# Optimization experiments

Measured on AMD Instinct MI355X. Metric: run time of the kernel, lower is better.

The kernel has to match this reference:

```python
import jax, jax.numpy as jnp
import numpy as np
from jax import lax

B, N, C, CN, M, H, W = 2, 8192, 64, 64, 16, 180, 240
LN_EPS = 1e-5  # torch nn.LayerNorm([C]) default eps


def setup_inputs():
    key = jax.random.key(0)
    ks = jax.random.split(key, 20)
    x = jax.random.uniform(ks[0], (B, N)) * (W - 1)
    y = jax.random.uniform(ks[1], (B, N)) * (H - 1)
    t = jax.random.uniform(ks[2], (B, N))
    p = jnp.where(jax.random.uniform(ks[3], (B, N)) < 0.5, -1.0, 1.0)
    events = jnp.stack([x, y, t, p], axis=-1)  # [B,N,4]
    s = 0.05
    w = lambda k, shape: jax.random.normal(k, shape) * s
    return {
        "events": events,
        "W_mlp1": w(ks[4], (4, C)),
        "W_pe": w(ks[5], (4, CN)),
        "ln_w": jnp.ones((C,)),
        "ln_b": jnp.zeros((C,)),
        "lx_Wq": w(ks[6], (C, CN)), "lx_Wk": w(ks[7], (C, CN)),
        "lx_Wv": w(ks[8], (C, CN)), "lx_Wsa1": w(ks[9], (CN, 1)),
        "lx_Wsa2": w(ks[10], (CN, C)),
        "gx_Wq": w(ks[11], (C, CN)), "gx_Wk": w(ks[12], (C, CN)),
        "gx_Wv": w(ks[13], (C, CN)), "gx_Wpe": w(ks[14], (C, CN)),
        "gx_Wsa1": w(ks[15], (CN, 1)), "gx_Wsa2": w(ks[16], (CN, C)),
    }


def select_nearest(vect, m):
    # torch: F.pad(left=m//2, right=m//2-1) then unfold(dim=1, size=m, step=1)
    b, n, c = vect.shape
    pad = m // 2
    vp = jnp.pad(vect, ((0, 0), (pad, pad - 1), (0, 0)))
    idx = jnp.arange(n)[:, None] + jnp.arange(m)[None, :]  # [N,M]
    return vp[:, idx, :]  # [B,N,M,C]


def fps(event, npoint):
    # faithful farthest_point_sample_batch; masked_select returns the sampled
    # points in ORIGINAL index order, hence the sort of selected indices.
    b, n, c = event.shape
    bary = jnp.mean(event, axis=1, keepdims=True)
    farthest0 = jnp.argmax(jnp.sum((event - bary) ** 2, -1), axis=1)  # [B]
    dist0 = jnp.full((b, n), 1e10, event.dtype)

    def step(carry, _):
        distance, farthest = carry
        centroid = jnp.take_along_axis(event, farthest[:, None, None], axis=1)
        d = jnp.sum((event - centroid) ** 2, -1)
        distance = jnp.minimum(distance, d)  # distance[dist<distance]=dist
        return (distance, jnp.argmax(distance, axis=1)), farthest

    _, sel = lax.scan(step, (dist0, farthest0), None, length=npoint)
    sel = jnp.sort(sel.T, axis=1)  # [B,npoint], sorted index order
    return jnp.take_along_axis(event, sel[:, :, None], axis=1)  # [B,npoint,C]


def sub_attention(q, k_multi, v_multi, pe, Wsa1, Wsa2):
    # sa = q - k + pe -> Linear(Cn,1) -> softmax over M.
    # The original then computes matmul(scores[B,1,N,M], (v+pe)^T[B,Cn,M,N])
    # and sums over the last axis, which is exactly
    #   scores @ (sum_n (v_multi + pe))  -- computed here without the
    # [B,Cn,N,N] intermediate.
    sa = q[:, :, None, :] - k_multi + pe          # [B,N,M,Cn]
    logits = jnp.squeeze(sa @ Wsa1, -1)           # [B,N,M]
    scores = jax.nn.softmax(logits, axis=-1)
    S = jnp.sum(v_multi + pe, axis=1)             # [B,M,Cn]
    p_attn = jnp.einsum("bnm,bmc->bnc", scores, S)
    return p_attn @ Wsa2                          # [B,N,C]


def layer_norm(x, w, b):
    mu = jnp.mean(x, axis=-1, keepdims=True)
    var = jnp.var(x, axis=-1, keepdims=True)
    return (x - mu) / jnp.sqrt(var + LN_EPS) * w + b


def normalize_nonzero(space):
    # mean/std over nonzero entries (std unbiased, ddof=1 as torch.std)
    mask = space != 0
    cnt = jnp.sum(mask)
    mean = jnp.sum(jnp.where(mask, space, 0.0)) / jnp.maximum(cnt, 1)
    var = jnp.sum(jnp.where(mask, (space - mean) ** 2, 0.0)) / jnp.maximum(cnt - 1, 1)
    std = jnp.sqrt(var)
    centered = jnp.where(mask, space - mean, space)
    safe_std = jnp.where(std > 0, std, 1.0)
    normed = jnp.where(std > 0, centered / safe_std, centered)
    return jnp.where(cnt > 0, normed, space)


def events_to_image(feat, ev, ln_w, ln_b):
    # feat [N,C], ev [N,4]
    h = jax.nn.gelu(layer_norm(feat, ln_w, ln_b), approximate=False)
    xi = jnp.floor(ev[:, 0]).astype(jnp.int32)
    yi = jnp.floor(ev[:, 1]).astype(jnp.int32)
    p = ev[:, 3]
    flat = yi * W + xi
    space = jnp.zeros((H * W, h.shape[1]), h.dtype).at[flat].add(p[:, None] * h)
    return normalize_nonzero(space.reshape(H, W, -1))


def reference(events, W_mlp1, W_pe, ln_w, ln_b,
              lx_Wq, lx_Wk, lx_Wv, lx_Wsa1, lx_Wsa2,
              gx_Wq, gx_Wk, gx_Wv, gx_Wpe, gx_Wsa1, gx_Wsa2):
    b, n, _ = events.shape
    lx_in = events @ W_mlp1                                    # [B,N,C]
    # EventTransformer position encoding: unfold-neighbor differences in raw
    # 4-d event space, then Linear(4,Cn)
    pe = (events[:, :, None, :] - select_nearest(events, M)) @ W_pe  # [B,N,M,Cn]
    # LXformer
    q = lx_in @ lx_Wq
    k = lx_in @ lx_Wk
    v = lx_in @ lx_Wv
    lx_sa = sub_attention(q, select_nearest(k, M), select_nearest(v, M),
                          pe, lx_Wsa1, lx_Wsa2)
    lx_out = lx_in + lx_sa
    # GXformer: FPS-sampled global keys/values, FPS-based position encoding
    pe_g = (lx_out[:, :, None, :] - fps(lx_out, M)[:, None, :, :]) @ gx_Wpe
    qg = lx_out @ gx_Wq
    kg = lx_out @ gx_Wk
    vg = lx_out @ gx_Wv
    k_m = jnp.broadcast_to(fps(kg, M)[:, None], (b, n, M, CN))
    v_m = jnp.broadcast_to(fps(vg, M)[:, None], (b, n, M, CN))
    gx_sa = sub_attention(qg, k_m, v_m, pe_g, gx_Wsa1, gx_Wsa2)
    gx_out = lx_out + gx_sa
    # scatter events to image per batch element
    imgs = jax.vmap(lambda f, e: events_to_image(f, e, ln_w, ln_b))(gx_out, events)
    return jnp.transpose(imgs, (0, 3, 1, 2))  # [B,C,H,W]
```

## Files before the change

kernel.cpp:

```cpp
#include <hip/hip_runtime.h>


typedef unsigned short u16;
typedef unsigned long long ull;

#define NB 8192
#define IMG_H 180
#define IMG_W 240
#define HWPIX (IMG_H*IMG_W)
#define SPB (HWPIX*64)
#define NC (NB*64)

#define TT_AC    0
#define TT_T     16384
#define TT_W1    32768
#define TT_EDGEV 32960
#define TT_EDGEF 35008
#define TT_S     37056
#define TT_SEL   39104
#define TT_CG    45248
#define TT_ESUM  45376
#define TT_STATS 45408
#define TT_SYNC  45440
#define TT_GCNT  45632
#define TT_LXS   45664
#define TT_ZOFF  45376
#define TT_ZCNT  416
#define TT_TOT   45792

__device__ __forceinline__ float bf2f(u16 u){
  union { unsigned int i; float f; } w; w.i = ((unsigned int)u) << 16; return w.f;
}
__device__ __forceinline__ u16 f2bf(float f){
  union { unsigned int i; float f; } w; w.f = f;
  unsigned int x = w.i;
  x += 0x7fffu + ((x >> 16) & 1u);
  return (u16)(x >> 16);
}
__device__ __forceinline__ bool isbf(const void* ev){
  unsigned w3 = ((const unsigned*)ev)[3];
  return !(w3 == 0x3F800000u || w3 == 0xBF800000u);
}
__device__ __forceinline__ float ld(const void* p, int i, bool bf){
  return bf ? bf2f(((const u16*)p)[i]) : ((const float*)p)[i];
}
__device__ __forceinline__ void stout(void* o, long i, float v, bool bf){
  if (bf) ((u16*)o)[i] = f2bf(v); else ((float*)o)[i] = v;
}
__device__ __forceinline__ float waveSum(float v){
#pragma unroll
  for (int m = 1; m < 64; m <<= 1) v += __shfl_xor(v, m, 64);
  return v;
}
__device__ __forceinline__ ull waveMaxU64(ull v){
#pragma unroll
  for (int m = 1; m < 64; m <<= 1){
    ull o = (ull)__shfl_xor((long long)v, m, 64);
    if (o > v) v = o;
  }
  return v;
}
__device__ __forceinline__ ull packPDI(int phase, float d, int n){
  return ((ull)phase << 45) | ((ull)__float_as_uint(d) << 13) | (ull)(8191 - n);
}
__device__ __forceinline__ int unpackI(ull p){ return 8191 - (int)(p & 0x1FFFull); }

__global__ void kW(const void* __restrict__ ev, const void* __restrict__ Wq,
                   const void* __restrict__ Wk, const void* __restrict__ Wpe,
                   const void* __restrict__ w1, float* __restrict__ ws, int tail){
  const bool bf = isbf(ev);
  const int tid = threadIdx.x;
  for (int i = tid; i < TT_ZCNT; i += 256) ws[tail + TT_ZOFF + i] = 0.f;
  if (tid < 64){
    float s1 = 0.f, s2 = 0.f;
    for (int c = 0; c < 64; c++){
      float wc = ld(w1, c, bf);
      s1 += ld(Wq, tid*64 + c, bf) * wc;
      s2 += ld(Wk, tid*64 + c, bf) * wc;
    }
    ws[tail + TT_W1 + tid] = s1;
    ws[tail + TT_W1 + 64 + tid] = s2;
    if (tid < 4){
      float s3 = 0.f;
      for (int c = 0; c < 64; c++) s3 += ld(Wpe, tid*64 + c, bf) * ld(w1, c, bf);
      ws[tail + TT_W1 + 128 + tid] = s3;
    }
  }
}

__global__ void __launch_bounds__(256, 4) kA(const void* __restrict__ ev,
    const void* __restrict__ Wm, const void* __restrict__ Wpe,
    const void* __restrict__ Wv, float* __restrict__ ws,
    int offA, int strA, int tail, int bb0){
  const bool bf = isbf(ev);
  const int bb = bb0 + blockIdx.z;
  const int lane = threadIdx.x & 63, w = threadIdx.x >> 6;
  float* A = ws + offA + (size_t)bb*strA;
  const float wq1 = ws[tail + TT_W1 + lane];
  const float wk1 = ws[tail + TT_W1 + 64 + lane];
  const float wp10 = ws[tail+TT_W1+128], wp11 = ws[tail+TT_W1+129],
              wp12 = ws[tail+TT_W1+130], wp13 = ws[tail+TT_W1+131];
  const float wm0 = ld(Wm, 0*64+lane, bf), wm1 = ld(Wm, 1*64+lane, bf),
              wm2 = ld(Wm, 2*64+lane, bf), wm3 = ld(Wm, 3*64+lane, bf);
  const bool edgeBlk = (blockIdx.x == 0 || blockIdx.x == 1023);
  float se0 = 0.f, se1 = 0.f, se2 = 0.f, se3 = 0.f;
#pragma unroll
  for (int i = 0; i < 2; i++){
    const int n = blockIdx.x*8 + w + 4*i;
    const int e4 = (bb*NB + n)*4;
    float e0 = ld(ev, e4+0, bf), e1 = ld(ev, e4+1, bf),
          e2 = ld(ev, e4+2, bf), e3 = ld(ev, e4+3, bf);
    se0 += e0; se1 += e1; se2 += e2; se3 += e3;
    float lx = e0*wm0 + e1*wm1 + e2*wm2 + e3*wm3;
    float epe = e0*wp10 + e1*wp11 + e2*wp12 + e3*wp13;
    float acv = waveSum(lx * wq1) + epe;
    float tv  = waveSum(lx * wk1) + epe;
    A[n*64 + lane] = lx;
    if (lane == 0){
      ws[tail + TT_AC + bb*8192 + n] = acv;
      ws[tail + TT_T  + bb*8192 + n] = tv;
    }
    if (edgeBlk && (n < 8 || n >= NB-8)){
      int e = (n < 8) ? n : (n - (NB-16));
      float v = 0.f;
      for (int cn = 0; cn < 64; cn++)
        v += __shfl(lx, cn, 64) * ld(Wv, cn*64 + lane, bf);
      float f = e0*ld(Wpe, lane, bf) + e1*ld(Wpe, 64+lane, bf)
              + e2*ld(Wpe, 128+lane, bf) + e3*ld(Wpe, 192+lane, bf);
      ws[tail + TT_EDGEV + bb*1024 + e*64 + lane] = v;
      ws[tail + TT_EDGEF + bb*1024 + e*64 + lane] = f;
    }
  }
  __shared__ float esum[4][4];
  if (lane == 0){ esum[w][0]=se0; esum[w][1]=se1; esum[w][2]=se2; esum[w][3]=se3; }
  __syncthreads();
  if (threadIdx.x < 4)
    atomicAdd(&ws[tail + TT_ESUM + bb*16 + threadIdx.x],
              esum[0][threadIdx.x]+esum[1][threadIdx.x]+esum[2][threadIdx.x]+esum[3][threadIdx.x]);
}

__global__ void __launch_bounds__(64) kB(const void* __restrict__ ev,
    const void* __restrict__ Wm, const void* __restrict__ Wv,
    const void* __restrict__ Wsa2, float* __restrict__ ws, int tail, int bb0){
  const bool bf = isbf(ev);
  const int bb = bb0 + blockIdx.z;
  const int m = blockIdx.x, lane = threadIdx.x;
  float tm = 0.f;
#pragma unroll
  for (int i = 0; i < 4; i++) tm += ws[tail + TT_ESUM + bb*16 + i] * ld(Wm, i*64 + lane, bf);
  float vs0 = 0.f, vs1 = 0.f;
#pragma unroll
  for (int j = 0; j < 64; j += 2){
    vs0 += __shfl(tm, j, 64)   * ld(Wv, j*64 + lane, bf);
    vs1 += __shfl(tm, j+1, 64) * ld(Wv, (j+1)*64 + lane, bf);
  }
  float vsum = vs0 + vs1;
  const int d = m - 8;
  float sv = 0.f, sf = 0.f;
  const float* EV = ws + tail + TT_EDGEV + bb*1024;
  const float* EF = ws + tail + TT_EDGEF + bb*1024;
  if (d < 0){
    for (int e = 16 + d; e < 16; e++){ sv += EV[e*64+lane]; sf += EF[e*64+lane]; }
  } else {
    for (int e = 0; e < d; e++){ sv += EV[e*64+lane]; sf += EF[e*64+lane]; }
  }
  float S = vsum - sv + sf;
  float sw0 = 0.f, sw1 = 0.f;
#pragma unroll
  for (int c = 0; c < 64; c += 2){
    sw0 += __shfl(S, c, 64)   * ld(Wsa2, c*64 + lane, bf);
    sw1 += __shfl(S, c+1, 64) * ld(Wsa2, (c+1)*64 + lane, bf);
  }
  ws[tail + TT_S + bb*1024 + m*64 + lane] = sw0 + sw1;
}

__global__ void __launch_bounds__(256) kC(const void* __restrict__ ev,
    const void* __restrict__ gWk, const void* __restrict__ gWv,
    float* __restrict__ ws,
    int offA, int strA, int offB, int strB, int offC, int strC,
    int tail, int bb0){
  const bool bf = isbf(ev);
  const int bb = bb0 + blockIdx.z;
  float* A = ws + offA + (size_t)bb*strA;
  float* Bp = ws + offB + (size_t)bb*strB;
  float* Cp = ws + offC + (size_t)bb*strC;
  __shared__ float SW_lds[1024];
  __shared__ float WK[4096];
  __shared__ float WV[4096];
  __shared__ float lred[4][64];
  const int tid = threadIdx.x, lane = tid & 63, w = tid >> 6;
  for (int i = tid; i < 1024; i += 256) SW_lds[i] = ws[tail + TT_S + bb*1024 + i];
  for (int i = tid; i < 4096; i += 256){
    WK[i] = ld(gWk, i, bf);
    WV[i] = ld(gWv, i, bf);
  }
  __syncthreads();
  float lxoR[2];
  float lxsum = 0.f;
#pragma unroll
  for (int i = 0; i < 2; i++){
    const int n = blockIdx.x*8 + w + 4*i;
    float lx  = A[n*64 + lane];
    float acn = ws[tail + TT_AC + bb*8192 + n];
    const int m = lane & 15;
    const int j = n + m - 8;
    float tv = (j >= 0 && j < NB) ? ws[tail + TT_T + bb*8192 + j] : 0.f;
    float logit = acn - tv;
    float mx = logit;
#pragma unroll
    for (int k = 1; k < 16; k <<= 1) mx = fmaxf(mx, __shfl_xor(mx, k, 64));
    float ex = expf(logit - mx);
    float sm = ex;
#pragma unroll
    for (int k = 1; k < 16; k <<= 1) sm += __shfl_xor(sm, k, 64);
    float sig = ex / sm;
    float sa = 0.f;
#pragma unroll
    for (int mm = 0; mm < 16; mm++) sa += __shfl(sig, mm, 64) * SW_lds[mm*64 + lane];
    float lxo = lx + sa;
    lxoR[i] = lxo;
    Bp[n*64 + lane] = lxo;
    lxsum += lxo;
  }
  lred[w][lane] = lxsum;
#pragma unroll
  for (int i = 0; i < 2; i++){
    const int n = blockIdx.x*8 + w + 4*i;
    float k0 = 0.f, k1 = 0.f, v0 = 0.f, v1 = 0.f;
#pragma unroll
    for (int cn = 0; cn < 64; cn += 2){
      float x0 = __shfl(lxoR[i], cn, 64);
      float x1 = __shfl(lxoR[i], cn+1, 64);
      k0 += x0 * WK[cn*64 + lane];
      k1 += x1 * WK[(cn+1)*64 + lane];
      v0 += x0 * WV[cn*64 + lane];
      v1 += x1 * WV[(cn+1)*64 + lane];
    }
    A[n*64 + lane] = k0 + k1;
    Cp[n*64 + lane] = v0 + v1;
  }
  __syncthreads();
  if (tid < 64)
    atomicAdd(&ws[tail + TT_LXS + bb*64 + tid],
              lred[0][tid]+lred[1][tid]+lred[2][tid]+lred[3][tid]);
}

__global__ void __launch_bounds__(512) kFPS(const void* __restrict__ ev,
    const void* __restrict__ gWk, const void* __restrict__ gWv,
    const void* __restrict__ gWpe, const void* __restrict__ gWsa1,
    const void* __restrict__ gWsa2, float* __restrict__ ws,
    int offA, int strA, int offB, int strB, int offC, int strC,
    int tail, int bb0){
  const int g = blockIdx.y, idx = blockIdx.x;
  const int bb = bb0 + blockIdx.z;
  const int tid = threadIdx.x, lane = tid & 63, w = tid >> 6;
  const float* pts = ws + (g == 0 ? offB + (size_t)bb*strB
                         : g == 1 ? offA + (size_t)bb*strA
                                  : offC + (size_t)bb*strC);
  ull* slot = (ull*)(ws + tail + TT_SYNC + (bb*3 + g)*32);
  int* gcnt = (int*)(ws + tail + TT_GCNT + bb*16);

  __shared__ float cent[64];
  __shared__ float lxsS[64];
  __shared__ ull   wvS[8];
  __shared__ int   selS[16];
  __shared__ int   sCur;
  __shared__ float gfS[1024];
  __shared__ float betaS[16];
  __shared__ float GS[64];

  const int n0 = idx*1024 + tid;
  float4 P[2][16];
#pragma unroll
  for (int j = 0; j < 2; j++)
#pragma unroll
    for (int i = 0; i < 16; i++)
      P[j][i] = ((const float4*)(pts + (size_t)(n0 + j*512)*64))[i];

  const bool bf = isbf(ev);
  if (tid < 64){
    float lxs = ws[tail + TT_LXS + bb*64 + tid];
    lxsS[tid] = lxs;
    float c;
    if (g == 0) c = lxs * (1.0f/NB);
    else {
      const void* W = (g == 1) ? gWk : gWv;
      float s = 0.f;
#pragma unroll
      for (int j = 0; j < 64; j++) s += __shfl(lxs, j, 64) * ld(W, j*64 + tid, bf);
      c = s * (1.0f/NB);
    }
    cent[tid] = c;
  }
  __syncthreads();

  const float4* cv = (const float4*)cent;
  float md[2] = {1e10f, 1e10f};
  int cur;

  {
    float dd[2];
#pragma unroll
    for (int j = 0; j < 2; j++){
      float d = 0.f;
#pragma unroll
      for (int i = 0; i < 16; i++){
        float4 c = cv[i];
        float dx = P[j][i].x-c.x, dy = P[j][i].y-c.y, dz = P[j][i].z-c.z, dw = P[j][i].w-c.w;
        d += dx*dx; d += dy*dy; d += dz*dz; d += dw*dw;
      }
      dd[j] = d;
    }
    ull p0 = packPDI(1, dd[0], n0);
    ull p1 = packPDI(1, dd[1], n0 + 512);
    ull bp = waveMaxU64(p0 > p1 ? p0 : p1);
    if (lane == 0) wvS[w] = bp;
    __syncthreads();
    if (w == 0){
      ull v = (lane < 8) ? wvS[lane] : 0;
#pragma unroll
      for (int m = 1; m < 8; m <<= 1){
        ull o = (ull)__shfl_xor((long long)v, m, 64);
        if (o > v) v = o;
      }
      if (lane == 0)
        __hip_atomic_store(&slot[8 + idx], v, __ATOMIC_RELEASE, __HIP_MEMORY_SCOPE_AGENT);
      ull got;
      for (;;){
        got = (lane < 8) ? __hip_atomic_load(&slot[8 + lane], __ATOMIC_RELAXED, __HIP_MEMORY_SCOPE_AGENT) : 0;
        ull ok = __ballot(lane >= 8 || (int)(got >> 45) == 1);
        if (ok == ~0ull) break;
        __builtin_amdgcn_s_sleep(1);
      }
#pragma unroll
      for (int m = 1; m < 8; m <<= 1){
        ull o = (ull)__shfl_xor((long long)got, m, 64);
        if (o > got) got = o;
      }
      if (lane == 0) sCur = unpackI(got);
    }
    __syncthreads();
    cur = sCur;
  }

  for (int it = 0; ; it++){
    if (tid == 0) selS[it] = cur;
    if (it == 15) break;
    if (tid < 16) ((float4*)cent)[tid] = ((const float4*)(pts + (size_t)cur*64))[tid];
    __syncthreads();
    const int phase = it + 2;
    float dd[2];
#pragma unroll
    for (int j = 0; j < 2; j++){
      float d = 0.f;
#pragma unroll
      for (int i = 0; i < 16; i++){
        float4 c = cv[i];
        float dx = P[j][i].x-c.x, dy = P[j][i].y-c.y, dz = P[j][i].z-c.z, dw = P[j][i].w-c.w;
        d += dx*dx; d += dy*dy; d += dz*dz; d += dw*dw;
      }
      md[j] = fminf(md[j], d);
      dd[j] = md[j];
    }
    ull p0 = packPDI(phase, dd[0], n0);
    ull p1 = packPDI(phase, dd[1], n0 + 512);
    ull bp = waveMaxU64(p0 > p1 ? p0 : p1);
    if (lane == 0) wvS[w] = bp;
    __syncthreads();
    const int par = phase & 1;
    if (w == 0){
      ull v = (lane < 8) ? wvS[lane] : 0;
#pragma unroll
      for (int m = 1; m < 8; m <<= 1){
        ull o = (ull)__shfl_xor((long long)v, m, 64);
        if (o > v) v = o;
      }
      if (lane == 0)
        __hip_atomic_store(&slot[par*8 + idx], v, __ATOMIC_RELEASE, __HIP_MEMORY_SCOPE_AGENT);
      ull got;
      for (;;){
        got = (lane < 8) ? __hip_atomic_load(&slot[par*8 + lane], __ATOMIC_RELAXED, __HIP_MEMORY_SCOPE_AGENT) : 0;
        ull ok = __ballot(lane >= 8 || (int)(got >> 45) == phase);
        if (ok == ~0ull) break;
        __builtin_amdgcn_s_sleep(1);
      }
#pragma unroll
      for (int m = 1; m < 8; m <<= 1){
        ull o = (ull)__shfl_xor((long long)got, m, 64);
        if (o > got) got = o;
      }
      if (lane == 0) sCur = unpackI(got);
    }
    __syncthreads();
    cur = sCur;
  }
  __syncthreads();

  if (idx == 0){
    if (tid == 0){
      for (int i = 1; i < 16; i++){
        int key = selS[i]; int j = i - 1;
        while (j >= 0 && selS[j] > key){ selS[j+1] = selS[j]; j--; }
        selS[j+1] = key;
      }
    }
    __syncthreads();
    for (int idx2 = tid; idx2 < 1024; idx2 += 512)
      ws[tail + TT_SEL + bb*3072 + g*1024 + idx2] = pts[(size_t)selS[idx2 >> 6]*64 + (idx2 & 63)];
    __threadfence();
  }
  __syncthreads();
  if (tid == 0) atomicAdd(gcnt, 1);
  if (g != 0 || idx != 0) return;

  if (tid == 0){
    while (__hip_atomic_load(gcnt, __ATOMIC_RELAXED, __HIP_MEMORY_SCOPE_AGENT) < 24)
      __builtin_amdgcn_s_sleep(1);
    __threadfence();
  }
  __syncthreads();
  if (tid < 64){
    const float gw1 = ld(gWsa1, tid, bf);
    float wpec[64];
#pragma unroll
    for (int cn = 0; cn < 64; cn++) wpec[cn] = ld(gWpe, cn*64 + tid, bf);
    float lxs = lxsS[tid];
    float G = 0.f;
#pragma unroll
    for (int cn = 0; cn < 64; cn++) G += __shfl(lxs, cn, 64) * wpec[cn];
    GS[tid] = G;
    const float* selp = ws + tail + TT_SEL + bb*3072;
    for (int m = 0; m < 16; m++){
      float plx = selp[m*64 + tid];
      float g2 = 0.f;
#pragma unroll
      for (int cn = 0; cn < 64; cn++) g2 += __shfl(plx, cn, 64) * wpec[cn];
      gfS[m*64 + tid] = g2;
      float pkv = selp[1024 + m*64 + tid];
      float part = waveSum((pkv + g2) * gw1);
      if (tid == 0) betaS[m] = part;
    }
  }
  __syncthreads();
  if (tid < 64){
    float mx = -1e30f;
    for (int m = 0; m < 16; m++) mx = fmaxf(mx, -betaS[m]);
    float ssum = 0.f;
    for (int m = 0; m < 16; m++) ssum += expf(-betaS[m] - mx);
    float A = 0.f;
    for (int m = 0; m < 16; m++){
      float sg = expf(-betaS[m] - mx) / ssum;
      float pv = ws[tail + TT_SEL + bb*3072 + 2048 + m*64 + tid];
      float Sg = 8192.0f * (pv - gfS[m*64 + tid]) + GS[tid];
      A += sg * Sg;
    }
    float cg = 0.f;
#pragma unroll
    for (int cn = 0; cn < 64; cn++) cg += __shfl(A, cn, 64) * ld(gWsa2, cn*64 + tid, bf);
    ws[tail + TT_CG + bb*64 + tid] = cg;
  }
}

__global__ void kZeroSpace(float* __restrict__ ws, int offSp, int strSp, int bb0){
  const int bb = bb0 + blockIdx.z;
  float4 z = make_float4(0.f, 0.f, 0.f, 0.f);
  ((float4*)(ws + offSp + (size_t)bb*strSp))[blockIdx.x*256 + threadIdx.x] = z;
}

__global__ void __launch_bounds__(256, 4) kImg(const void* __restrict__ ev,
    const void* __restrict__ lnw, const void* __restrict__ lnb,
    float* __restrict__ ws, int offB, int strB, int offSp, int strSp,
    int tail, int bb0){
  const bool bf = isbf(ev);
  const int bb = bb0 + blockIdx.z;
  const int lane = threadIdx.x & 63, w = threadIdx.x >> 6;
  const float cg = ws[tail + TT_CG + bb*64 + lane];
  const float lw = ld(lnw, lane, bf), lb = ld(lnb, lane, bf);
  float* space = ws + offSp + (size_t)bb*strSp;
  const float* Bp = ws + offB + (size_t)bb*strB;
#pragma unroll
  for (int i = 0; i < 2; i++){
    const int n = blockIdx.x*8 + w + 4*i;
    float x = Bp[n*64 + lane] + cg;
    float mu = waveSum(x) * (1.0f/64.0f);
    float dv = x - mu;
    float var = waveSum(dv*dv) * (1.0f/64.0f);
    float xn = dv / sqrtf(var + 1e-5f);
    float y = xn * lw + lb;
    float h = 0.5f * y * (1.0f + erff(y * 0.70710678118654752f));
    const int e4 = (bb*NB + n)*4;
    float exf = ld(ev, e4+0, bf), eyf = ld(ev, e4+1, bf), epf = ld(ev, e4+3, bf);
    int xi = (int)floorf(exf), yi = (int)floorf(eyf);
    int flat = yi*IMG_W + xi;
    flat = max(0, min(HWPIX-1, flat));
    atomicAdd(space + flat*64 + lane, epf * h);
  }
}

__global__ void __launch_bounds__(256) kStat(float* __restrict__ ws,
    int offSp, int strSp, int tail, int bb0){
  const int bb = bb0 + blockIdx.z;
  const float4* sp = (const float4*)(ws + offSp + (size_t)bb*strSp);
  float cnt = 0.f, sum = 0.f, ssq = 0.f;
  for (unsigned i = blockIdx.x*256u + threadIdx.x; i < SPB/4; i += 65536u){
    float4 v = sp[i];
    if (v.x != 0.f){ cnt += 1.f; sum += v.x; ssq += v.x*v.x; }
    if (v.y != 0.f){ cnt += 1.f; sum += v.y; ssq += v.y*v.y; }
    if (v.z != 0.f){ cnt += 1.f; sum += v.z; ssq += v.z*v.z; }
    if (v.w != 0.f){ cnt += 1.f; sum += v.w; ssq += v.w*v.w; }
  }
  cnt = waveSum(cnt); sum = waveSum(sum); ssq = waveSum(ssq);
  __shared__ float rc[4], rs[4], rq[4];
  const int lane = threadIdx.x & 63, w = threadIdx.x >> 6;
  if (lane == 0){ rc[w] = cnt; rs[w] = sum; rq[w] = ssq; }
  __syncthreads();
  if (threadIdx.x == 0){
    atomicAdd(&ws[tail + TT_STATS + bb*16 + 0], rc[0]+rc[1]+rc[2]+rc[3]);
    atomicAdd(&ws[tail + TT_STATS + bb*16 + 1], rs[0]+rs[1]+rs[2]+rs[3]);
    atomicAdd(&ws[tail + TT_STATS + bb*16 + 2], rq[0]+rq[1]+rq[2]+rq[3]);
  }
}

__global__ void __launch_bounds__(256) kOut(const void* __restrict__ ev,
    const float* __restrict__ ws, void* __restrict__ out,
    int offSp, int strSp, int tail, int bb0){
  const bool bf = isbf(ev);
  const int bb = bb0 + blockIdx.z;
  __shared__ float tile[64*65];
  const int tid = threadIdx.x;
  const int hw0 = blockIdx.x*64;
  const float* sp = ws + offSp + (size_t)bb*strSp;
#pragma unroll
  for (int i = 0; i < 16; i++){
    int idx = tid + 256*i;
    tile[(idx >> 6)*65 + (idx & 63)] = sp[(size_t)hw0*64 + idx];
  }
  const float cnt = ws[tail + TT_STATS + bb*16 + 0];
  const float sum = ws[tail + TT_STATS + bb*16 + 1];
  const float ssq = ws[tail + TT_STATS + bb*16 + 2];
  const float mean = sum / fmaxf(cnt, 1.f);
  const float m2   = fmaxf(ssq - sum*mean, 0.f);
  const float var  = m2 / fmaxf(cnt - 1.f, 1.f);
  const float stdv = sqrtf(var);
  __syncthreads();
  const int c = tid >> 2, sub = tid & 3;
#pragma unroll
  for (int j = 0; j < 16; j++){
    int hwl = sub*16 + j;
    float x = tile[hwl*65 + c];
    float centered = (x != 0.f) ? (x - mean) : x;
    float normed = (stdv > 0.f) ? (centered / stdv) : centered;
    float o = (cnt > 0.f) ? normed : x;
    stout(out, (long)(bb*64 + c)*HWPIX + hw0 + hwl, o, bf);
  }
}

extern "C" void kernel_launch(void* const* d_in, const int* in_sizes, int n_in,
                              void* d_out, int out_size, void* d_ws, size_t ws_size,
                              hipStream_t stream){
  (void)in_sizes; (void)n_in; (void)out_size;
  const void* ev     = d_in[0];
  const void* Wm     = d_in[1];
  const void* Wpe    = d_in[2];
  const void* lnw    = d_in[3];
  const void* lnb    = d_in[4];
  const void* lxWq   = d_in[5];
  const void* lxWk   = d_in[6];
  const void* lxWv   = d_in[7];
  const void* lxWsa1 = d_in[8];
  const void* lxWsa2 = d_in[9];
  const void* gxWk   = d_in[11];
  const void* gxWv   = d_in[12];
  const void* gxWpe  = d_in[13];
  const void* gxWsa1 = d_in[14];
  const void* gxWsa2 = d_in[15];
  float* ws = (float*)d_ws;

  const int P_TAIL = 2*NC + 2*SPB;
  const size_t PAR_BYTES = (size_t)(P_TAIL + TT_TOT) * 4;
  const bool par = ws_size >= PAR_BYTES;

  int offB, strB, offSp, strSp, offA, strA, offC, strC, tail;
  if (par){
    offB = 0;        strB = NC;
    offSp = 2*NC;    strSp = SPB;
    offA = 2*NC;     strA = NC;
    offC = 4*NC;     strC = NC;
    tail = P_TAIL;
  } else {
    offSp = 0;       strSp = 0;
    offA = 0;        strA = 0;
    offC = NC;       strC = 0;
    offB = SPB;      strB = 0;
    tail = SPB + NC;
  }
  const int nb = par ? 2 : 1;
  const int iters = par ? 1 : 2;

  kW<<<1, 256, 0, stream>>>(ev, lxWq, lxWk, Wpe, lxWsa1, ws, tail);
  for (int t = 0; t < iters; t++){
    const int bb0 = par ? 0 : t;
    kA<<<dim3(1024,1,nb), 256, 0, stream>>>(ev, Wm, Wpe, lxWv, ws, offA, strA, tail, bb0);
    kB<<<dim3(16,1,nb), 64, 0, stream>>>(ev, Wm, lxWv, lxWsa2, ws, tail, bb0);
    kC<<<dim3(1024,1,nb), 256, 0, stream>>>(ev, gxWk, gxWv, ws,
        offA, strA, offB, strB, offC, strC, tail, bb0);
    kFPS<<<dim3(8,3,nb), 512, 0, stream>>>(ev, gxWk, gxWv, gxWpe, gxWsa1, gxWsa2, ws,
        offA, strA, offB, strB, offC, strC, tail, bb0);
    kZeroSpace<<<dim3(2700,1,nb), 256, 0, stream>>>(ws, offSp, strSp, bb0);
    kImg<<<dim3(1024,1,nb), 256, 0, stream>>>(ev, lnw, lnb, ws, offB, strB, offSp, strSp, tail, bb0);
    kStat<<<dim3(256,1,nb), 256, 0, stream>>>(ws, offSp, strSp, tail, bb0);
    kOut<<<dim3(675,1,nb), 256, 0, stream>>>(ev, ws, d_out, offSp, strSp, tail, bb0);
  }
}
```

Baseline: 327.9 us.

## Fuse image stats into output kernel and overlap space zeroing with FPS

The separate statistics pass is merged into the output kernel: each block gathers partial count, sum and sum-of-squares from its tile, and all blocks then meet at a spin-wait grid barrier on a global counter. This removes one full read of the image buffer. Most of the image-buffer zeroing moves into an extra grid slice of the FPS launch, so it runs while FPS is working. Only the part that aliases live buffers is zeroed afterwards. kC now passes activations through LDS with float4 reads instead of wave shuffles. The spin barrier assumes all 675 blocks per batch are resident at once, which risks deadlock, and the arrival counter is never visibly reset.

```diff
diff --git a/kernel.cpp b/kernel.cpp
--- a/kernel.cpp
+++ b/kernel.cpp
@@ -187,19 +187,21 @@
   __shared__ float SW_lds[1024];
   __shared__ float WK[4096];
   __shared__ float WV[4096];
-  __shared__ float lred[4][64];
+  __shared__ __align__(16) float LXU[8*64 + 8*16];
   const int tid = threadIdx.x, lane = tid & 63, w = tid >> 6;
+  float* LX  = LXU;
+  float* SIG = LXU + 512;
   for (int i = tid; i < 1024; i += 256) SW_lds[i] = ws[tail + TT_S + bb*1024 + i];
   for (int i = tid; i < 4096; i += 256){
     WK[i] = ld(gWk, i, bf);
     WV[i] = ld(gWv, i, bf);
   }
   __syncthreads();
-  float lxoR[2];
   float lxsum = 0.f;
 #pragma unroll
   for (int i = 0; i < 2; i++){
-    const int n = blockIdx.x*8 + w + 4*i;
+    const int p = w + 4*i;
+    const int n = blockIdx.x*8 + p;
     float lx  = A[n*64 + lane];
     float acn = ws[tail + TT_AC + bb*8192 + n];
     const int m = lane & 15;
@@ -214,35 +216,42 @@
 #pragma unroll
     for (int k = 1; k < 16; k <<= 1) sm += __shfl_xor(sm, k, 64);
     float sig = ex / sm;
+    if (lane < 16) SIG[p*16 + lane] = sig;
     float sa = 0.f;
 #pragma unroll
-    for (int mm = 0; mm < 16; mm++) sa += __shfl(sig, mm, 64) * SW_lds[mm*64 + lane];
+    for (int mm = 0; mm < 16; mm += 4){
+      float4 s4 = *(const float4*)&SIG[p*16 + mm];
+      sa += s4.x*SW_lds[ mm   *64+lane] + s4.y*SW_lds[(mm+1)*64+lane]
+          + s4.z*SW_lds[(mm+2)*64+lane] + s4.w*SW_lds[(mm+3)*64+lane];
+    }
     float lxo = lx + sa;
-    lxoR[i] = lxo;
+    LX[p*64 + lane] = lxo;
     Bp[n*64 + lane] = lxo;
     lxsum += lxo;
   }
-  lred[w][lane] = lxsum;
 #pragma unroll
   for (int i = 0; i < 2; i++){
-    const int n = blockIdx.x*8 + w + 4*i;
-    float k0 = 0.f, k1 = 0.f, v0 = 0.f, v1 = 0.f;
-#pragma unroll
-    for (int cn = 0; cn < 64; cn += 2){
-      float x0 = __shfl(lxoR[i], cn, 64);
-      float x1 = __shfl(lxoR[i], cn+1, 64);
-      k0 += x0 * WK[cn*64 + lane];
-      k1 += x1 * WK[(cn+1)*64 + lane];
-      v0 += x0 * WV[cn*64 + lane];
-      v1 += x1 * WV[(cn+1)*64 + lane];
-    }
-    A[n*64 + lane] = k0 + k1;
-    Cp[n*64 + lane] = v0 + v1;
-  }
+    const int p = w + 4*i;
+    const int n = blockIdx.x*8 + p;
+    float k0 = 0.f, v0 = 0.f;
+#pragma unroll
+    for (int cn = 0; cn < 64; cn += 4){
+      float4 x4 = *(const float4*)&LX[p*64 + cn];
+      k0 += x4.x*WK[ cn   *64+lane] + x4.y*WK[(cn+1)*64+lane]
+          + x4.z*WK[(cn+2)*64+lane] + x4.w*WK[(cn+3)*64+lane];
+      v0 += x4.x*WV[ cn   *64+lane] + x4.y*WV[(cn+1)*64+lane]
+          + x4.z*WV[(cn+2)*64+lane] + x4.w*WV[(cn+3)*64+lane];
+    }
+    A[n*64 + lane] = k0;
+    Cp[n*64 + lane] = v0;
+  }
+  __syncthreads();
+  float* lred = LXU;
+  lred[w*64 + lane] = lxsum;
   __syncthreads();
   if (tid < 64)
     atomicAdd(&ws[tail + TT_LXS + bb*64 + tid],
-              lred[0][tid]+lred[1][tid]+lred[2][tid]+lred[3][tid]);
+              lred[tid]+lred[64+tid]+lred[128+tid]+lred[192+tid]);
 }
 
 __global__ void __launch_bounds__(512) kFPS(const void* __restrict__ ev,
@@ -250,10 +259,21 @@
     const void* __restrict__ gWpe, const void* __restrict__ gWsa1,
     const void* __restrict__ gWsa2, float* __restrict__ ws,
     int offA, int strA, int offB, int strB, int offC, int strC,
-    int tail, int bb0){
+    int offSp, int strSp, int tail, int bb0){
   const int g = blockIdx.y, idx = blockIdx.x;
   const int bb = bb0 + blockIdx.z;
   const int tid = threadIdx.x, lane = tid & 63, w = tid >> 6;
+
+  if (g == 3){
+    float4 z = make_float4(0.f, 0.f, 0.f, 0.f);
+    size_t base; unsigned cnt4;
+    if (blockIdx.z == 0){ base = (size_t)offSp + 4u*NC; cnt4 = (SPB - 4*NC)/4; }
+    else                { base = (size_t)offSp + (size_t)strSp; cnt4 = SPB/4; }
+    float4* p = (float4*)(ws + base);
+    for (unsigned i = idx*512u + tid; i < cnt4; i += 8u*512u) p[i] = z;
+    return;
+  }
+
   const float* pts = ws + (g == 0 ? offB + (size_t)bb*strB
                          : g == 1 ? offA + (size_t)bb*strA
                                   : offC + (size_t)bb*strC);
@@ -461,10 +481,10 @@
   }
 }
 
-__global__ void kZeroSpace(float* __restrict__ ws, int offSp, int strSp, int bb0){
-  const int bb = bb0 + blockIdx.z;
-  float4 z = make_float4(0.f, 0.f, 0.f, 0.f);
-  ((float4*)(ws + offSp + (size_t)bb*strSp))[blockIdx.x*256 + threadIdx.x] = z;
+__global__ void kZero(float* __restrict__ ws, int base, unsigned count4){
+  unsigned i = blockIdx.x*256u + threadIdx.x;
+  if (i < count4)
+    ((float4*)(ws + base))[i] = make_float4(0.f, 0.f, 0.f, 0.f);
 }
 
 __global__ void __launch_bounds__(256, 4) kImg(const void* __restrict__ ev,
@@ -497,52 +517,51 @@
   }
 }
 
-__global__ void __launch_bounds__(256) kStat(float* __restrict__ ws,
-    int offSp, int strSp, int tail, int bb0){
-  const int bb = bb0 + blockIdx.z;
-  const float4* sp = (const float4*)(ws + offSp + (size_t)bb*strSp);
-  float cnt = 0.f, sum = 0.f, ssq = 0.f;
-  for (unsigned i = blockIdx.x*256u + threadIdx.x; i < SPB/4; i += 65536u){
-    float4 v = sp[i];
-    if (v.x != 0.f){ cnt += 1.f; sum += v.x; ssq += v.x*v.x; }
-    if (v.y != 0.f){ cnt += 1.f; sum += v.y; ssq += v.y*v.y; }
-    if (v.z != 0.f){ cnt += 1.f; sum += v.z; ssq += v.z*v.z; }
-    if (v.w != 0.f){ cnt += 1.f; sum += v.w; ssq += v.w*v.w; }
-  }
-  cnt = waveSum(cnt); sum = waveSum(sum); ssq = waveSum(ssq);
-  __shared__ float rc[4], rs[4], rq[4];
-  const int lane = threadIdx.x & 63, w = threadIdx.x >> 6;
-  if (lane == 0){ rc[w] = cnt; rs[w] = sum; rq[w] = ssq; }
-  __syncthreads();
-  if (threadIdx.x == 0){
-    atomicAdd(&ws[tail + TT_STATS + bb*16 + 0], rc[0]+rc[1]+rc[2]+rc[3]);
-    atomicAdd(&ws[tail + TT_STATS + bb*16 + 1], rs[0]+rs[1]+rs[2]+rs[3]);
-    atomicAdd(&ws[tail + TT_STATS + bb*16 + 2], rq[0]+rq[1]+rq[2]+rq[3]);
-  }
-}
-
-__global__ void __launch_bounds__(256) kOut(const void* __restrict__ ev,
-    const float* __restrict__ ws, void* __restrict__ out,
-    int offSp, int strSp, int tail, int bb0){
+__global__ void __launch_bounds__(256) kOut2(const void* __restrict__ ev,
+    float* __restrict__ ws, void* __restrict__ out,
+    int offSp, int strSp, int tail, int bb0, int nArrive){
   const bool bf = isbf(ev);
   const int bb = bb0 + blockIdx.z;
   __shared__ float tile[64*65];
-  const int tid = threadIdx.x;
+  __shared__ float rc[4], rs[4], rq[4];
+  __shared__ float sStats[3];
+  const int tid = threadIdx.x, lane = tid & 63, w = tid >> 6;
   const int hw0 = blockIdx.x*64;
   const float* sp = ws + offSp + (size_t)bb*strSp;
+  float cnt = 0.f, sum = 0.f, ssq = 0.f;
 #pragma unroll
   for (int i = 0; i < 16; i++){
     int idx = tid + 256*i;
-    tile[(idx >> 6)*65 + (idx & 63)] = sp[(size_t)hw0*64 + idx];
-  }
-  const float cnt = ws[tail + TT_STATS + bb*16 + 0];
-  const float sum = ws[tail + TT_STATS + bb*16 + 1];
-  const float ssq = ws[tail + TT_STATS + bb*16 + 2];
-  const float mean = sum / fmaxf(cnt, 1.f);
-  const float m2   = fmaxf(ssq - sum*mean, 0.f);
-  const float var  = m2 / fmaxf(cnt - 1.f, 1.f);
+    float x = sp[(size_t)hw0*64 + idx];
+    tile[(idx >> 6)*65 + (idx & 63)] = x;
+    if (x != 0.f){ cnt += 1.f; sum += x; ssq += x*x; }
+  }
+  cnt = waveSum(cnt); sum = waveSum(sum); ssq = waveSum(ssq);
+  if (lane == 0){ rc[w] = cnt; rs[w] = sum; rq[w] = ssq; }
+  __syncthreads();
+  float* ST = ws + tail + TT_STATS + bb*16;
+  int* cntr = (int*)(ws + tail + TT_GCNT + bb*16 + 8);
+  if (tid == 0){
+    atomicAdd(&ST[0], rc[0]+rc[1]+rc[2]+rc[3]);
+    atomicAdd(&ST[1], rs[0]+rs[1]+rs[2]+rs[3]);
+    atomicAdd(&ST[2], rq[0]+rq[1]+rq[2]+rq[3]);
+    __threadfence();
+    atomicAdd(cntr, 1);
+    while (__hip_atomic_load(cntr, __ATOMIC_RELAXED, __HIP_MEMORY_SCOPE_AGENT) < nArrive)
+      __builtin_amdgcn_s_sleep(2);
+    __threadfence();
+    sStats[0] = __hip_atomic_load(&ST[0], __ATOMIC_RELAXED, __HIP_MEMORY_SCOPE_AGENT);
+    sStats[1] = __hip_atomic_load(&ST[1], __ATOMIC_RELAXED, __HIP_MEMORY_SCOPE_AGENT);
+    sStats[2] = __hip_atomic_load(&ST[2], __ATOMIC_RELAXED, __HIP_MEMORY_SCOPE_AGENT);
+  }
+  __syncthreads();
+  const float cntf = sStats[0];
+  const float sumf = sStats[1];
+  const float ssqf = sStats[2];
+  const float mean = sumf / fmaxf(cntf, 1.f);
+  const float m2   = fmaxf(ssqf - sumf*mean, 0.f);
+  const float var  = m2 / fmaxf(cntf - 1.f, 1.f);
   const float stdv = sqrtf(var);
-  __syncthreads();
   const int c = tid >> 2, sub = tid & 3;
 #pragma unroll
   for (int j = 0; j < 16; j++){
@@ -550,7 +569,7 @@
     float x = tile[hwl*65 + c];
     float centered = (x != 0.f) ? (x - mean) : x;
     float normed = (stdv > 0.f) ? (centered / stdv) : centered;
-    float o = (cnt > 0.f) ? normed : x;
+    float o = (cntf > 0.f) ? normed : x;
     stout(out, (long)(bb*64 + c)*HWPIX + hw0 + hwl, o, bf);
   }
 }
@@ -604,11 +623,13 @@
     kB<<<dim3(16,1,nb), 64, 0, stream>>>(ev, Wm, lxWv, lxWsa2, ws, tail, bb0);
     kC<<<dim3(1024,1,nb), 256, 0, stream>>>(ev, gxWk, gxWv, ws,
         offA, strA, offB, strB, offC, strC, tail, bb0);
-    kFPS<<<dim3(8,3,nb), 512, 0, stream>>>(ev, gxWk, gxWv, gxWpe, gxWsa1, gxWsa2, ws,
-        offA, strA, offB, strB, offC, strC, tail, bb0);
-    kZeroSpace<<<dim3(2700,1,nb), 256, 0, stream>>>(ws, offSp, strSp, bb0);
+    kFPS<<<dim3(8, par ? 4 : 3, nb), 512, 0, stream>>>(ev, gxWk, gxWv, gxWpe, gxWsa1, gxWsa2, ws,
+        offA, strA, offB, strB, offC, strC, offSp, strSp, tail, bb0);
+    if (par)
+      kZero<<<dim3(2048,1,1), 256, 0, stream>>>(ws, offSp, (unsigned)NC);
+    else
+      kZero<<<dim3(2700,1,1), 256, 0, stream>>>(ws, offSp, (unsigned)(SPB/4));
     kImg<<<dim3(1024,1,nb), 256, 0, stream>>>(ev, lnw, lnb, ws, offB, strB, offSp, strSp, tail, bb0);
-    kStat<<<dim3(256,1,nb), 256, 0, stream>>>(ws, offSp, strSp, tail, bb0);
-    kOut<<<dim3(675,1,nb), 256, 0, stream>>>(ev, ws, d_out, offSp, strSp, tail, bb0);
-  }
-}
+    kOut2<<<dim3(675,1,nb), 256, 0, stream>>>(ev, ws, d_out, offSp, strSp, tail, bb0, 675);
+  }
+}
```

Result: slower. 475.9 us (+45.1%).
